# Kernel optimization log

Hardware: AMD Instinct MI355X
Metric: run time of the kernel (lower is better)

The kernel has to match this reference:

```python
import jax, jax.numpy as jnp
import numpy as np

EPS = 1e-5
ALPHA = 0.2  # leaky relu negative slope


def instance_norm(x):
    # x: [b, n, c]; torch InstanceNorm1d normalizes each (b, c) over the n dim (no affine)
    mean = jnp.mean(x, axis=1, keepdims=True)
    var = jnp.var(x, axis=1, keepdims=True)
    return (x - mean) * jax.lax.rsqrt(var + EPS)


def gat_layer(x, w, a_src, a_dst, bias):
    # x: [b, n, f_in], w: [h, f_in, f_out], a_src/a_dst: [h, f_out, 1], bias: [f_out]
    h_prime = jnp.einsum('bnf,hfo->bhno', x, w)              # [b, h, n, f_out]
    attn_src = jnp.einsum('bhno,hoi->bhni', h_prime, a_src)[..., 0]  # [b, h, n]
    attn_dst = jnp.einsum('bhno,hoi->bhni', h_prime, a_dst)[..., 0]  # [b, h, n]
    # outer-sum additive attention: attn[b,h,i,j] = src[b,h,i] + dst[b,h,j]
    attn = attn_src[:, :, :, None] + attn_dst[:, :, None, :]
    attn = jnp.where(attn >= 0, attn, ALPHA * attn)          # leaky relu
    attn = jax.nn.softmax(attn, axis=-1)
    out = jnp.einsum('bhnm,bhmo->bhno', attn, h_prime) + bias
    return out


def setup_inputs() -> dict:
    key = jax.random.key(0)
    ks = jax.random.split(key, 9)
    b, n = 16, 1024
    f0, f1, f2 = 32, 16, 32   # n_units
    h0, h1 = 4, 1             # n_heads

    def xavier(k, shape, gain=1.414):
        fan_in, fan_out = shape[-2], shape[-1]
        a = gain * np.sqrt(6.0 / (fan_in + fan_out))
        return jax.random.uniform(k, shape, jnp.float32, -a, a)

    return {
        'x': jax.random.normal(ks[0], (b, n, f0), jnp.float32),
        'w1': xavier(ks[1], (h0, f0, f1)),
        'a_src1': xavier(ks[2], (h0, f1, 1)),
        'a_dst1': xavier(ks[3], (h0, f1, 1)),
        'b1': jnp.zeros((f1,), jnp.float32),
        'w2': xavier(ks[4], (h1, f1 * h0, f2)),
        'a_src2': xavier(ks[5], (h1, f2, 1)),
        'a_dst2': xavier(ks[6], (h1, f2, 1)),
        'b2': jnp.zeros((f2,), jnp.float32),
    }


def reference(x, w1, a_src1, a_dst1, b1, w2, a_src2, a_dst2, b2):
    b, n = x.shape[:2]
    # layer 0
    x = instance_norm(x)
    out = gat_layer(x, w1, a_src1, a_dst1, b1)               # [b, h0, n, f1]
    x = jnp.transpose(out, (0, 2, 1, 3)).reshape(b, n, -1)   # [b, n, h0*f1]
    x = jax.nn.elu(x)
    # layer 1 (last): squeeze head dim
    x = instance_norm(x)
    out = gat_layer(x, w2, a_src2, a_dst2, b2)               # [b, 1, n, f2]
    return out[:, 0]                                          # [b, n, f2]
```

## Files before the change

### kernel.cpp

```cpp
#include <hip/hip_runtime.h>


namespace {
constexpr int Nn  = 1024;
constexpr int F0  = 32;
constexpr int F1n = 16;
constexpr int FH  = 64;
constexpr int F2n = 32;
constexpr float LOG2E = 1.4426950408889634f;
constexpr float EPS   = 1e-5f;
constexpr float ALPHA = 0.2f;
}

typedef __attribute__((ext_vector_type(8))) _Float16 half8;
typedef __attribute__((ext_vector_type(4))) float f32x4;

__global__ __launch_bounds__(1024) void k_stats1(
    const float* __restrict__ x, float* __restrict__ stats)
{
  const int b = blockIdx.x;
  const int t = threadIdx.x;
  const int c = t & 31, seg = t >> 5;

  __shared__ float s_sum[32][33];
  __shared__ float s_ssq[32][33];

  const float* xb = x + (size_t)b * Nn * F0;
  float sum = 0.f, ssq = 0.f;
#pragma unroll 4
  for (int k = 0; k < 32; k++) {
    float v = xb[(seg * 32 + k) * F0 + c];
    sum += v; ssq += v * v;
  }
  s_sum[seg][c] = sum; s_ssq[seg][c] = ssq;
  __syncthreads();
  if (t < 32) {
    float s = 0.f, q = 0.f;
#pragma unroll
    for (int k = 0; k < 32; k++) { s += s_sum[k][t]; q += s_ssq[k][t]; }
    const float mean = s * (1.f / Nn);
    const float var  = fmaf(-mean, mean, q * (1.f / Nn));
    stats[b * 64 + t]      = mean;
    stats[b * 64 + 32 + t] = rsqrtf(var + EPS);
  }
}

__global__ __launch_bounds__(256, 4) void k_proj1(
    const float* __restrict__ x, const float* __restrict__ stats,
    const float* __restrict__ w1,
    const float* __restrict__ asrc, const float* __restrict__ adst,
    short* __restrict__ hpT_hi, short* __restrict__ hpT_lo,
    float* __restrict__ src, float* __restrict__ dst)
{
  const int b    = blockIdx.x >> 4;
  const int tile = blockIdx.x & 15;
  const int t    = threadIdx.x;
  const int r    = t & 63, h = t >> 6;

  __shared__ float s_x[64 * 33];
  __shared__ float s_wt[4 * F1n * F0];
  __shared__ float s_mean[32], s_rstd[32];
  __shared__ float s_as[64], s_ad[64];

  const float* xb = x + (size_t)b * Nn * F0 + (size_t)tile * 64 * F0;
  for (int idx = t; idx < 64 * F0; idx += 256) {
    const int rr = idx >> 5, f = idx & 31;
    s_x[rr * 33 + f] = xb[idx];
  }
  for (int idx = t; idx < 4 * F1n * F0; idx += 256) {
    const int f = idx & 31, ho = idx >> 5;
    s_wt[idx] = w1[((ho >> 4) * F0 + f) * F1n + (ho & 15)];
  }
  if (t < 32)                 s_mean[t] = stats[b * 64 + t];
  else if (t < 64)            s_rstd[t - 32] = stats[b * 64 + t];
  if (t < 64) { s_as[t] = asrc[t]; s_ad[t] = adst[t]; }
  __syncthreads();
  for (int idx = t; idx < 64 * F0; idx += 256) {
    const int rr = idx >> 5, f = idx & 31;
    s_x[rr * 33 + f] = (s_x[rr * 33 + f] - s_mean[f]) * s_rstd[f];
  }
  __syncthreads();

  const int n    = tile * 64 + r;
  const int bh   = b * 4 + h;
  float sdot = 0.f, ddot = 0.f;
#pragma unroll 1
  for (int o = 0; o < F1n; o++) {
    float acc = 0.f;
#pragma unroll
    for (int f = 0; f < F0; f++)
      acc = fmaf(s_x[r * 33 + f], s_wt[(h * F1n + o) * F0 + f], acc);
    sdot = fmaf(acc, s_as[h * F1n + o], sdot);
    ddot = fmaf(acc, s_ad[h * F1n + o], ddot);
    const _Float16 hh = (_Float16)acc;
    const _Float16 hl = (_Float16)(acc - (float)hh);
    const size_t idx = ((size_t)bh * F1n + o) * Nn + n;
    hpT_hi[idx] = __builtin_bit_cast(short, hh);
    hpT_lo[idx] = __builtin_bit_cast(short, hl);
  }
  src[bh * Nn + n] = sdot;
  dst[bh * Nn + n] = ddot;
}

__global__ __launch_bounds__(256) void k_attn1(
    const short* __restrict__ hpT_hi, const short* __restrict__ hpT_lo,
    const float* __restrict__ src, const float* __restrict__ dst,
    const float* __restrict__ bias, float* __restrict__ x1)
{
  const int bh   = blockIdx.x >> 4;
  const int tile = blockIdx.x & 15;
  const int t    = threadIdx.x;
  const int w    = t >> 6;
  const int l    = t & 63;
  const int col  = l & 15;
  const int ks   = l >> 4;

  __shared__ float s_dst[Nn];
  __shared__ float s_red[4];
  __shared__ float s_ps[4][16];

  const float* dp = dst + bh * Nn;
  float lm = -1e30f;
  for (int j = t; j < Nn; j += 256) { float v = dp[j]; s_dst[j] = v; lm = fmaxf(lm, v); }
#pragma unroll
  for (int mask = 32; mask >= 1; mask >>= 1) lm = fmaxf(lm, __shfl_xor(lm, mask));
  if (l == 0) s_red[w] = lm;
  __syncthreads();
  const float dmax = fmaxf(fmaxf(s_red[0], s_red[1]), fmaxf(s_red[2], s_red[3]));

  const int i0 = tile * 64 + w * 16;
  const float si = src[bh * Nn + i0 + col];
  const float t0v = si + dmax;
  const float em  = fmaxf(t0v, ALPHA * t0v) * LOG2E;

  auto pexp = [&](float dv) {
    const float tt = si + dv;
    const float u  = fmaxf(tt, ALPHA * tt);
    return exp2f(fmaf(u, LOG2E, -em));
  };

  const half8* bph = reinterpret_cast<const half8*>(hpT_hi + (size_t)bh * F1n * Nn);
  const half8* bpl = reinterpret_cast<const half8*>(hpT_lo + (size_t)bh * F1n * Nn);
  f32x4 acc = {0.f, 0.f, 0.f, 0.f};
  float psum = 0.f;

#pragma unroll 2
  for (int jb = 0; jb < 32; ++jb) {
    const int jo = (jb << 5) | (ks << 3);
    const float4 dA = *reinterpret_cast<const float4*>(&s_dst[jo]);
    const float4 dB = *reinterpret_cast<const float4*>(&s_dst[jo + 4]);
    half8 af;
    const _Float16 q0 = (_Float16)pexp(dA.x); af[0] = q0;
    const _Float16 q1 = (_Float16)pexp(dA.y); af[1] = q1;
    const _Float16 q2 = (_Float16)pexp(dA.z); af[2] = q2;
    const _Float16 q3 = (_Float16)pexp(dA.w); af[3] = q3;
    const _Float16 q4 = (_Float16)pexp(dB.x); af[4] = q4;
    const _Float16 q5 = (_Float16)pexp(dB.y); af[5] = q5;
    const _Float16 q6 = (_Float16)pexp(dB.z); af[6] = q6;
    const _Float16 q7 = (_Float16)pexp(dB.w); af[7] = q7;
    psum += (((float)q0 + (float)q1) + ((float)q2 + (float)q3)) +
            (((float)q4 + (float)q5) + ((float)q6 + (float)q7));

    const half8 bh8 = bph[col * 128 + (jb << 2) + ks];
    const half8 bl8 = bpl[col * 128 + (jb << 2) + ks];
    acc = __builtin_amdgcn_mfma_f32_16x16x32_f16(af, bh8, acc, 0, 0, 0);
    acc = __builtin_amdgcn_mfma_f32_16x16x32_f16(af, bl8, acc, 0, 0, 0);
  }

  psum += __shfl_xor(psum, 16);
  psum += __shfl_xor(psum, 32);
  if (l < 16) s_ps[w][col] = psum;
  __syncthreads();

  const int b = bh >> 2, h = bh & 3;
  const float bc = bias[col];
#pragma unroll
  for (int r = 0; r < 4; ++r) {
    const int row = ks * 4 + r;
    const float inv = 1.f / s_ps[w][row];
    float v = fmaf(acc[r], inv, bc);
    v = v > 0.f ? v : exp2f(v * LOG2E) - 1.f;
    x1[((size_t)(b * Nn + i0 + row)) * FH + h * F1n + col] = v;
  }
}

__global__ __launch_bounds__(1024) void k_stats2(
    const float* __restrict__ x1, float* __restrict__ stats)
{
  const int b = blockIdx.x;
  const int t = threadIdx.x;
  const int c = t & 63, seg = t >> 6;

  __shared__ float s_sum[16][65];
  __shared__ float s_ssq[16][65];

  const float* xb = x1 + (size_t)b * Nn * FH;
  float sum = 0.f, ssq = 0.f;
#pragma unroll 4
  for (int k = 0; k < 64; k++) {
    float v = xb[(seg * 64 + k) * FH + c];
    sum += v; ssq += v * v;
  }
  s_sum[seg][c] = sum; s_ssq[seg][c] = ssq;
  __syncthreads();
  if (t < 64) {
    float s = 0.f, q = 0.f;
#pragma unroll
    for (int k = 0; k < 16; k++) { s += s_sum[k][t]; q += s_ssq[k][t]; }
    const float mean = s * (1.f / Nn);
    const float var  = fmaf(-mean, mean, q * (1.f / Nn));
    stats[b * 128 + t]      = mean;
    stats[b * 128 + 64 + t] = rsqrtf(var + EPS);
  }
}

__global__ __launch_bounds__(256, 4) void k_proj2(
    const float* __restrict__ x1, const float* __restrict__ stats,
    const float* __restrict__ w2,
    const float* __restrict__ asrc, const float* __restrict__ adst,
    short* __restrict__ hpT_hi, short* __restrict__ hpT_lo,
    float* __restrict__ src, float* __restrict__ dst)
{
  const int b    = blockIdx.x >> 4;
  const int tile = blockIdx.x & 15;
  const int t    = threadIdx.x;
  const int r    = t & 63, og = t >> 6;

  __shared__ float s_x[64 * 65];
  __shared__ float s_wt[F2n * FH];
  __shared__ float s_mean[64], s_rstd[64];
  __shared__ float s_as[F2n], s_ad[F2n];
  __shared__ float s_sd[4][64][2];

  const float* xb = x1 + (size_t)b * Nn * FH + (size_t)tile * 64 * FH;
  for (int idx = t; idx < 64 * FH; idx += 256) {
    const int rr = idx >> 6, f = idx & 63;
    s_x[rr * 65 + f] = xb[idx];
  }
  for (int idx = t; idx < F2n * FH; idx += 256) {
    const int f = idx & 63, o = idx >> 6;
    s_wt[idx] = w2[f * F2n + o];
  }
  if (t < 64)                 s_mean[t] = stats[b * 128 + t];
  else if (t < 128)           s_rstd[t - 64] = stats[b * 128 + t];
  if (t < F2n) { s_as[t] = asrc[t]; s_ad[t] = adst[t]; }
  __syncthreads();
  for (int idx = t; idx < 64 * FH; idx += 256) {
    const int rr = idx >> 6, f = idx & 63;
    s_x[rr * 65 + f] = (s_x[rr * 65 + f] - s_mean[f]) * s_rstd[f];
  }
  __syncthreads();

  const int n    = tile * 64 + r;
  const int base = b * Nn + n;
  float sdot = 0.f, ddot = 0.f;
#pragma unroll 1
  for (int oo = 0; oo < 8; oo++) {
    const int o = og * 8 + oo;
    float acc = 0.f;
#pragma unroll
    for (int f = 0; f < FH; f++)
      acc = fmaf(s_x[r * 65 + f], s_wt[o * FH + f], acc);
    sdot = fmaf(acc, s_as[o], sdot);
    ddot = fmaf(acc, s_ad[o], ddot);
    const _Float16 hh = (_Float16)acc;
    const _Float16 hl = (_Float16)(acc - (float)hh);
    const size_t idx = ((size_t)b * F2n + o) * Nn + n;
    hpT_hi[idx] = __builtin_bit_cast(short, hh);
    hpT_lo[idx] = __builtin_bit_cast(short, hl);
  }

  s_sd[og][r][0] = sdot; s_sd[og][r][1] = ddot;
  __syncthreads();
  if (og == 0) {
    float s = 0.f, d = 0.f;
#pragma unroll
    for (int g = 0; g < 4; g++) { s += s_sd[g][r][0]; d += s_sd[g][r][1]; }
    src[base] = s;
    dst[base] = d;
  }
}

__global__ __launch_bounds__(256) void k_attn2(
    const short* __restrict__ hpT_hi, const short* __restrict__ hpT_lo,
    const float* __restrict__ src, const float* __restrict__ dst,
    const float* __restrict__ bias, float* __restrict__ out)
{
  const int b    = blockIdx.x >> 6;
  const int tile = blockIdx.x & 63;
  const int t    = threadIdx.x;
  const int jq   = t >> 6;
  const int l    = t & 63;
  const int col  = l & 15;
  const int ks   = l >> 4;

  __shared__ float s_dst[Nn];
  __shared__ float s_red[4];
  __shared__ float s_comb[3][64][9];
  __shared__ float s_ps[16];

  const float* dp = dst + b * Nn;
  float lm = -1e30f;
  for (int j = t; j < Nn; j += 256) { float v = dp[j]; s_dst[j] = v; lm = fmaxf(lm, v); }
#pragma unroll
  for (int mask = 32; mask >= 1; mask >>= 1) lm = fmaxf(lm, __shfl_xor(lm, mask));
  if (l == 0) s_red[jq] = lm;
  __syncthreads();
  const float dmax = fmaxf(fmaxf(s_red[0], s_red[1]), fmaxf(s_red[2], s_red[3]));

  const int i0 = tile * 16;
  const float si = src[b * Nn + i0 + col];
  const float t0v = si + dmax;
  const float em  = fmaxf(t0v, ALPHA * t0v) * LOG2E;

  auto pexp = [&](float dv) {
    const float tt = si + dv;
    const float u  = fmaxf(tt, ALPHA * tt);
    return exp2f(fmaf(u, LOG2E, -em));
  };

  const half8* bph = reinterpret_cast<const half8*>(hpT_hi + (size_t)b * F2n * Nn);
  const half8* bpl = reinterpret_cast<const half8*>(hpT_lo + (size_t)b * F2n * Nn);
  f32x4 acc0 = {0.f, 0.f, 0.f, 0.f};
  f32x4 acc1 = {0.f, 0.f, 0.f, 0.f};
  float psum = 0.f;

#pragma unroll 2
  for (int kb = 0; kb < 8; ++kb) {
    const int jb = jq * 8 + kb;
    const int jo = (jb << 5) | (ks << 3);
    const float4 dA = *reinterpret_cast<const float4*>(&s_dst[jo]);
    const float4 dB = *reinterpret_cast<const float4*>(&s_dst[jo + 4]);
    half8 af;
    const _Float16 q0 = (_Float16)pexp(dA.x); af[0] = q0;
    const _Float16 q1 = (_Float16)pexp(dA.y); af[1] = q1;
    const _Float16 q2 = (_Float16)pexp(dA.z); af[2] = q2;
    const _Float16 q3 = (_Float16)pexp(dA.w); af[3] = q3;
    const _Float16 q4 = (_Float16)pexp(dB.x); af[4] = q4;
    const _Float16 q5 = (_Float16)pexp(dB.y); af[5] = q5;
    const _Float16 q6 = (_Float16)pexp(dB.z); af[6] = q6;
    const _Float16 q7 = (_Float16)pexp(dB.w); af[7] = q7;
    psum += (((float)q0 + (float)q1) + ((float)q2 + (float)q3)) +
            (((float)q4 + (float)q5) + ((float)q6 + (float)q7));

    const half8 bh0 = bph[col * 128 + (jb << 2) + ks];
    const half8 bl0 = bpl[col * 128 + (jb << 2) + ks];
    const half8 bh1 = bph[(col + 16) * 128 + (jb << 2) + ks];
    const half8 bl1 = bpl[(col + 16) * 128 + (jb << 2) + ks];
    acc0 = __builtin_amdgcn_mfma_f32_16x16x32_f16(af, bh0, acc0, 0, 0, 0);
    acc0 = __builtin_amdgcn_mfma_f32_16x16x32_f16(af, bl0, acc0, 0, 0, 0);
    acc1 = __builtin_amdgcn_mfma_f32_16x16x32_f16(af, bh1, acc1, 0, 0, 0);
    acc1 = __builtin_amdgcn_mfma_f32_16x16x32_f16(af, bl1, acc1, 0, 0, 0);
  }

  if (jq > 0) {
#pragma unroll
    for (int r = 0; r < 4; ++r) {
      s_comb[jq - 1][l][r]     = acc0[r];
      s_comb[jq - 1][l][r + 4] = acc1[r];
    }
    s_comb[jq - 1][l][8] = psum;
  }
  __syncthreads();

  if (jq == 0) {
#pragma unroll
    for (int g = 0; g < 3; ++g) {
#pragma unroll
      for (int r = 0; r < 4; ++r) {
        acc0[r] += s_comb[g][l][r];
        acc1[r] += s_comb[g][l][r + 4];
      }
      psum += s_comb[g][l][8];
    }
    psum += __shfl_xor(psum, 16);
    psum += __shfl_xor(psum, 32);
    if (l < 16) s_ps[col] = psum;

    const float bc0 = bias[col];
    const float bc1 = bias[col + 16];
#pragma unroll
    for (int r = 0; r < 4; ++r) {
      const int row = ks * 4 + r;
      const float inv = 1.f / s_ps[row];
      float* op = out + ((size_t)(b * Nn + i0 + row)) * F2n;
      op[col]      = fmaf(acc0[r], inv, bc0);
      op[col + 16] = fmaf(acc1[r], inv, bc1);
    }
  }
}

extern "C" void kernel_launch(void* const* d_in, const int* in_sizes, int n_in,
                              void* d_out, int out_size, void* d_ws, size_t ws_size,
                              hipStream_t stream) {
  (void)in_sizes; (void)n_in; (void)out_size; (void)ws_size;
  const float* x   = (const float*)d_in[0];
  const float* w1  = (const float*)d_in[1];
  const float* as1 = (const float*)d_in[2];
  const float* ad1 = (const float*)d_in[3];
  const float* b1  = (const float*)d_in[4];
  const float* w2  = (const float*)d_in[5];
  const float* as2 = (const float*)d_in[6];
  const float* ad2 = (const float*)d_in[7];
  const float* b2  = (const float*)d_in[8];
  float* out = (float*)d_out;

  float* ws = (float*)d_ws;
  short* hpT1_hi = (short*)ws;
  short* hpT1_lo = (short*)(ws + 524288);
  short* hpT2_hi = (short*)(ws + 1048576);
  short* hpT2_lo = (short*)(ws + 1048576 + 262144);
  float* x1      = ws + 1048576 + 524288;
  float* src1    = x1 + 1048576;
  float* dst1    = src1 + 65536;
  float* src2    = dst1 + 65536;
  float* dst2    = src2 + 16384;
  float* stats1  = dst2 + 16384;
  float* stats2  = stats1 + 1024;

  k_stats1<<<16, 1024, 0, stream>>>(x, stats1);
  k_proj1<<<256, 256, 0, stream>>>(x, stats1, w1, as1, ad1, hpT1_hi, hpT1_lo, src1, dst1);
  k_attn1<<<1024, 256, 0, stream>>>(hpT1_hi, hpT1_lo, src1, dst1, b1, x1);
  k_stats2<<<16, 1024, 0, stream>>>(x1, stats2);
  k_proj2<<<256, 256, 0, stream>>>(x1, stats2, w2, as2, ad2, hpT2_hi, hpT2_lo, src2, dst2);
  k_attn2<<<1024, 256, 0, stream>>>(hpT2_hi, hpT2_lo, src2, dst2, b2, out);
}
```

Baseline: 152.8 us.

## Fuse instance-norm statistics into projection and attention kernels, drop stats launches

Removes the two separate statistics kernels. Each layer-0 projection block now recomputes the full per-batch mean and variance of x itself (redundantly across 16 tiles). Layer-1 sum and sum-of-squares are accumulated with atomics in the attention-1 epilogue, and proj2 derives mean and rstd from them. The projection kernels also load rows straight into registers as float4 instead of staging through padded shared memory. This cuts two launches and a pass over x1, at the cost of redundant reads of x, atomic contention, and a less precise E[x^2]-mean^2 variance computed from fp32 atomic sums.

```diff
diff --git a/kernel.cpp b/kernel.cpp
--- a/kernel.cpp
+++ b/kernel.cpp
@@ -15,81 +15,81 @@
 typedef __attribute__((ext_vector_type(8))) _Float16 half8;
 typedef __attribute__((ext_vector_type(4))) float f32x4;
 
-__global__ __launch_bounds__(1024) void k_stats1(
-    const float* __restrict__ x, float* __restrict__ stats)
-{
-  const int b = blockIdx.x;
-  const int t = threadIdx.x;
-  const int c = t & 31, seg = t >> 5;
-
-  __shared__ float s_sum[32][33];
-  __shared__ float s_ssq[32][33];
-
-  const float* xb = x + (size_t)b * Nn * F0;
-  float sum = 0.f, ssq = 0.f;
-#pragma unroll 4
-  for (int k = 0; k < 32; k++) {
-    float v = xb[(seg * 32 + k) * F0 + c];
-    sum += v; ssq += v * v;
-  }
-  s_sum[seg][c] = sum; s_ssq[seg][c] = ssq;
-  __syncthreads();
-  if (t < 32) {
-    float s = 0.f, q = 0.f;
-#pragma unroll
-    for (int k = 0; k < 32; k++) { s += s_sum[k][t]; q += s_ssq[k][t]; }
-    const float mean = s * (1.f / Nn);
-    const float var  = fmaf(-mean, mean, q * (1.f / Nn));
-    stats[b * 64 + t]      = mean;
-    stats[b * 64 + 32 + t] = rsqrtf(var + EPS);
-  }
-}
-
-__global__ __launch_bounds__(256, 4) void k_proj1(
-    const float* __restrict__ x, const float* __restrict__ stats,
-    const float* __restrict__ w1,
+__global__ __launch_bounds__(256) void k_proj1(
+    const float* __restrict__ x, const float* __restrict__ w1,
     const float* __restrict__ asrc, const float* __restrict__ adst,
     short* __restrict__ hpT_hi, short* __restrict__ hpT_lo,
-    float* __restrict__ src, float* __restrict__ dst)
+    float* __restrict__ src, float* __restrict__ dst,
+    float* __restrict__ statsAcc)
 {
   const int b    = blockIdx.x >> 4;
   const int tile = blockIdx.x & 15;
   const int t    = threadIdx.x;
   const int r    = t & 63, h = t >> 6;
 
-  __shared__ float s_x[64 * 33];
-  __shared__ float s_wt[4 * F1n * F0];
-  __shared__ float s_mean[32], s_rstd[32];
-  __shared__ float s_as[64], s_ad[64];
-
-  const float* xb = x + (size_t)b * Nn * F0 + (size_t)tile * 64 * F0;
-  for (int idx = t; idx < 64 * F0; idx += 256) {
-    const int rr = idx >> 5, f = idx & 31;
-    s_x[rr * 33 + f] = xb[idx];
-  }
+  __shared__ float  s_sum[8][33];
+  __shared__ float  s_ssq[8][33];
+  __shared__ float  s_mean[32], s_rstd[32];
+  __shared__ float4 s_wt4[4 * F1n * (F0 / 4)];
+  __shared__ float  s_as[64], s_ad[64];
+
+  if (tile == 0 && t < 128) statsAcc[b * 128 + t] = 0.f;
+
+  float* s_wt = reinterpret_cast<float*>(s_wt4);
   for (int idx = t; idx < 4 * F1n * F0; idx += 256) {
     const int f = idx & 31, ho = idx >> 5;
     s_wt[idx] = w1[((ho >> 4) * F0 + f) * F1n + (ho & 15)];
   }
-  if (t < 32)                 s_mean[t] = stats[b * 64 + t];
-  else if (t < 64)            s_rstd[t - 32] = stats[b * 64 + t];
   if (t < 64) { s_as[t] = asrc[t]; s_ad[t] = adst[t]; }
-  __syncthreads();
-  for (int idx = t; idx < 64 * F0; idx += 256) {
-    const int rr = idx >> 5, f = idx & 31;
-    s_x[rr * 33 + f] = (s_x[rr * 33 + f] - s_mean[f]) * s_rstd[f];
-  }
-  __syncthreads();
-
-  const int n    = tile * 64 + r;
-  const int bh   = b * 4 + h;
+
+  const float* xb = x + (size_t)b * Nn * F0;
+  {
+    const int c = t & 31, seg = t >> 5;
+    float sum = 0.f, ssq = 0.f;
+#pragma unroll 8
+    for (int nn = seg; nn < Nn; nn += 8) {
+      float v = xb[nn * F0 + c];
+      sum += v; ssq += v * v;
+    }
+    s_sum[seg][c] = sum; s_ssq[seg][c] = ssq;
+  }
+  __syncthreads();
+  if (t < 32) {
+    float s = 0.f, q = 0.f;
+#pragma unroll
+    for (int k = 0; k < 8; k++) { s += s_sum[k][t]; q += s_ssq[k][t]; }
+    const float mean = s * (1.f / Nn);
+    const float var  = fmaf(-mean, mean, q * (1.f / Nn));
+    s_mean[t] = mean;
+    s_rstd[t] = rsqrtf(var + EPS);
+  }
+  __syncthreads();
+
+  const int n  = tile * 64 + r;
+  const int bh = b * 4 + h;
+  float4 xr[F0 / 4];
+  const float4* xrow = reinterpret_cast<const float4*>(xb + (size_t)n * F0);
+#pragma unroll
+  for (int k = 0; k < F0 / 4; k++) {
+    float4 v = xrow[k];
+    v.x = (v.x - s_mean[k * 4 + 0]) * s_rstd[k * 4 + 0];
+    v.y = (v.y - s_mean[k * 4 + 1]) * s_rstd[k * 4 + 1];
+    v.z = (v.z - s_mean[k * 4 + 2]) * s_rstd[k * 4 + 2];
+    v.w = (v.w - s_mean[k * 4 + 3]) * s_rstd[k * 4 + 3];
+    xr[k] = v;
+  }
+
   float sdot = 0.f, ddot = 0.f;
 #pragma unroll 1
   for (int o = 0; o < F1n; o++) {
     float acc = 0.f;
 #pragma unroll
-    for (int f = 0; f < F0; f++)
-      acc = fmaf(s_x[r * 33 + f], s_wt[(h * F1n + o) * F0 + f], acc);
+    for (int k = 0; k < F0 / 4; k++) {
+      const float4 wv = s_wt4[(h * F1n + o) * (F0 / 4) + k];
+      const float4 xv = xr[k];
+      acc = fmaf(xv.x, wv.x, acc); acc = fmaf(xv.y, wv.y, acc);
+      acc = fmaf(xv.z, wv.z, acc); acc = fmaf(xv.w, wv.w, acc);
+    }
     sdot = fmaf(acc, s_as[h * F1n + o], sdot);
     ddot = fmaf(acc, s_ad[h * F1n + o], ddot);
     const _Float16 hh = (_Float16)acc;
@@ -105,7 +105,8 @@
 __global__ __launch_bounds__(256) void k_attn1(
     const short* __restrict__ hpT_hi, const short* __restrict__ hpT_lo,
     const float* __restrict__ src, const float* __restrict__ dst,
-    const float* __restrict__ bias, float* __restrict__ x1)
+    const float* __restrict__ bias, float* __restrict__ x1,
+    float* __restrict__ statsAcc)
 {
   const int bh   = blockIdx.x >> 4;
   const int tile = blockIdx.x & 15;
@@ -174,6 +175,7 @@
 
   const int b = bh >> 2, h = bh & 3;
   const float bc = bias[col];
+  float sv = 0.f, sq = 0.f;
 #pragma unroll
   for (int r = 0; r < 4; ++r) {
     const int row = ks * 4 + r;
@@ -181,41 +183,19 @@
     float v = fmaf(acc[r], inv, bc);
     v = v > 0.f ? v : exp2f(v * LOG2E) - 1.f;
     x1[((size_t)(b * Nn + i0 + row)) * FH + h * F1n + col] = v;
-  }
-}
-
-__global__ __launch_bounds__(1024) void k_stats2(
-    const float* __restrict__ x1, float* __restrict__ stats)
-{
-  const int b = blockIdx.x;
-  const int t = threadIdx.x;
-  const int c = t & 63, seg = t >> 6;
-
-  __shared__ float s_sum[16][65];
-  __shared__ float s_ssq[16][65];
-
-  const float* xb = x1 + (size_t)b * Nn * FH;
-  float sum = 0.f, ssq = 0.f;
-#pragma unroll 4
-  for (int k = 0; k < 64; k++) {
-    float v = xb[(seg * 64 + k) * FH + c];
-    sum += v; ssq += v * v;
-  }
-  s_sum[seg][c] = sum; s_ssq[seg][c] = ssq;
-  __syncthreads();
-  if (t < 64) {
-    float s = 0.f, q = 0.f;
-#pragma unroll
-    for (int k = 0; k < 16; k++) { s += s_sum[k][t]; q += s_ssq[k][t]; }
-    const float mean = s * (1.f / Nn);
-    const float var  = fmaf(-mean, mean, q * (1.f / Nn));
-    stats[b * 128 + t]      = mean;
-    stats[b * 128 + 64 + t] = rsqrtf(var + EPS);
-  }
-}
-
-__global__ __launch_bounds__(256, 4) void k_proj2(
-    const float* __restrict__ x1, const float* __restrict__ stats,
+    sv += v; sq += v * v;
+  }
+  sv += __shfl_xor(sv, 16); sq += __shfl_xor(sq, 16);
+  sv += __shfl_xor(sv, 32); sq += __shfl_xor(sq, 32);
+  if (l < 16) {
+    const int ch = h * F1n + col;
+    atomicAdd(&statsAcc[b * 128 + ch], sv);
+    atomicAdd(&statsAcc[b * 128 + 64 + ch], sq);
+  }
+}
+
+__global__ __launch_bounds__(256) void k_proj2(
+    const float* __restrict__ x1, const float* __restrict__ statsAcc,
     const float* __restrict__ w2,
     const float* __restrict__ asrc, const float* __restrict__ adst,
     short* __restrict__ hpT_hi, short* __restrict__ hpT_lo,
@@ -226,41 +206,54 @@
   const int t    = threadIdx.x;
   const int r    = t & 63, og = t >> 6;
 
-  __shared__ float s_x[64 * 65];
-  __shared__ float s_wt[F2n * FH];
-  __shared__ float s_mean[64], s_rstd[64];
-  __shared__ float s_as[F2n], s_ad[F2n];
-  __shared__ float s_sd[4][64][2];
-
-  const float* xb = x1 + (size_t)b * Nn * FH + (size_t)tile * 64 * FH;
-  for (int idx = t; idx < 64 * FH; idx += 256) {
-    const int rr = idx >> 6, f = idx & 63;
-    s_x[rr * 65 + f] = xb[idx];
-  }
+  __shared__ float  s_mean[64], s_rstd[64];
+  __shared__ float4 s_wt4[F2n * (FH / 4)];
+  __shared__ float  s_as[F2n], s_ad[F2n];
+  __shared__ float  s_sd[4][64][2];
+
+  float* s_wt = reinterpret_cast<float*>(s_wt4);
   for (int idx = t; idx < F2n * FH; idx += 256) {
     const int f = idx & 63, o = idx >> 6;
     s_wt[idx] = w2[f * F2n + o];
   }
-  if (t < 64)                 s_mean[t] = stats[b * 128 + t];
-  else if (t < 128)           s_rstd[t - 64] = stats[b * 128 + t];
   if (t < F2n) { s_as[t] = asrc[t]; s_ad[t] = adst[t]; }
-  __syncthreads();
-  for (int idx = t; idx < 64 * FH; idx += 256) {
-    const int rr = idx >> 6, f = idx & 63;
-    s_x[rr * 65 + f] = (s_x[rr * 65 + f] - s_mean[f]) * s_rstd[f];
+  if (t < 64) {
+    const float s = statsAcc[b * 128 + t];
+    const float q = statsAcc[b * 128 + 64 + t];
+    const float mean = s * (1.f / Nn);
+    const float var  = fmaf(-mean, mean, q * (1.f / Nn));
+    s_mean[t] = mean;
+    s_rstd[t] = rsqrtf(var + EPS);
   }
   __syncthreads();
 
   const int n    = tile * 64 + r;
   const int base = b * Nn + n;
+  float4 xr[FH / 4];
+  const float4* xrow = reinterpret_cast<const float4*>(
+      x1 + (size_t)b * Nn * FH + (size_t)n * FH);
+#pragma unroll
+  for (int k = 0; k < FH / 4; k++) {
+    float4 v = xrow[k];
+    v.x = (v.x - s_mean[k * 4 + 0]) * s_rstd[k * 4 + 0];
+    v.y = (v.y - s_mean[k * 4 + 1]) * s_rstd[k * 4 + 1];
+    v.z = (v.z - s_mean[k * 4 + 2]) * s_rstd[k * 4 + 2];
+    v.w = (v.w - s_mean[k * 4 + 3]) * s_rstd[k * 4 + 3];
+    xr[k] = v;
+  }
+
   float sdot = 0.f, ddot = 0.f;
 #pragma unroll 1
   for (int oo = 0; oo < 8; oo++) {
     const int o = og * 8 + oo;
     float acc = 0.f;
 #pragma unroll
-    for (int f = 0; f < FH; f++)
-      acc = fmaf(s_x[r * 65 + f], s_wt[o * FH + f], acc);
+    for (int k = 0; k < FH / 4; k++) {
+      const float4 wv = s_wt4[o * (FH / 4) + k];
+      const float4 xv = xr[k];
+      acc = fmaf(xv.x, wv.x, acc); acc = fmaf(xv.y, wv.y, acc);
+      acc = fmaf(xv.z, wv.z, acc); acc = fmaf(xv.w, wv.w, acc);
+    }
     sdot = fmaf(acc, s_as[o], sdot);
     ddot = fmaf(acc, s_ad[o], ddot);
     const _Float16 hh = (_Float16)acc;
@@ -415,13 +408,10 @@
   float* dst1    = src1 + 65536;
   float* src2    = dst1 + 65536;
   float* dst2    = src2 + 16384;
-  float* stats1  = dst2 + 16384;
-  float* stats2  = stats1 + 1024;
-
-  k_stats1<<<16, 1024, 0, stream>>>(x, stats1);
-  k_proj1<<<256, 256, 0, stream>>>(x, stats1, w1, as1, ad1, hpT1_hi, hpT1_lo, src1, dst1);
-  k_attn1<<<1024, 256, 0, stream>>>(hpT1_hi, hpT1_lo, src1, dst1, b1, x1);
-  k_stats2<<<16, 1024, 0, stream>>>(x1, stats2);
-  k_proj2<<<256, 256, 0, stream>>>(x1, stats2, w2, as2, ad2, hpT2_hi, hpT2_lo, src2, dst2);
+  float* statsA  = dst2 + 16384;
+
+  k_proj1<<<256, 256, 0, stream>>>(x, w1, as1, ad1, hpT1_hi, hpT1_lo, src1, dst1, statsA);
+  k_attn1<<<1024, 256, 0, stream>>>(hpT1_hi, hpT1_lo, src1, dst1, b1, x1, statsA);
+  k_proj2<<<256, 256, 0, stream>>>(x1, statsA, w2, as2, ad2, hpT2_hi, hpT2_lo, src2, dst2);
   k_attn2<<<1024, 256, 0, stream>>>(hpT2_hi, hpT2_lo, src2, dst2, b2, out);
 }
```

After: 142.3 us (median of 2 runs). 6.8% less time.
